# Performance work log

Hardware: AMD Instinct MI355X
Metric: run time of the kernel (lower is better)

The kernel has to match this reference:

```python
import jax, jax.numpy as jnp
import numpy as np

EPS = 1e-5

def _ln(t, g, b):
    m = t.mean(-1, keepdims=True)
    v = ((t - m) ** 2).mean(-1, keepdims=True)
    return (t - m) * jax.lax.rsqrt(v + EPS) * g + b

def _sr(t, w, b, H, W, sr):
    # t: [B, H*W, C] -> spatial-reduction conv -> [B, (H//sr)*(W//sr), C]
    B, L, C = t.shape
    xi = t.transpose(0, 2, 1).reshape(B, C, H, W)
    y = jax.lax.conv_general_dilated(xi, w, (sr, sr), 'VALID',
                                     dimension_numbers=('NCHW', 'OIHW', 'NCHW'))
    return y.reshape(B, C, -1).transpose(0, 2, 1) + b

def setup_inputs() -> dict:
    key = jax.random.key(0)
    ks = jax.random.split(key, 9)
    C, head, sr, H, W = 128, 2, 2, 64, 64
    B, N = 4, 2 * H * W
    s = 0.02
    return {
        'x': jax.random.normal(ks[0], (B, N, C), jnp.float32),
        'qW': jax.random.normal(ks[1], (C, C), jnp.float32) * s,
        'qb': jnp.zeros((C,), jnp.float32),
        'kvW': jax.random.normal(ks[2], (C, 2 * C), jnp.float32) * s,
        'kvb': jnp.zeros((2 * C,), jnp.float32),
        'projW': jax.random.normal(ks[3], (C, C), jnp.float32) * s,
        'projb': jnp.zeros((C,), jnp.float32),
        'srW': jax.random.normal(ks[4], (C, C, sr, sr), jnp.float32) * s,
        'srb': jnp.zeros((C,), jnp.float32),
        'lnW': jnp.ones((C,), jnp.float32),
        'lnB': jnp.zeros((C,), jnp.float32),
        'H': H, 'W': W, 'fuse': 1,
    }

def reference(x, qW, qb, kvW, kvb, projW, projb, srW, srb, lnW, lnB, H, W, fuse):
    head, sr = 2, 2
    B, N, C = x.shape
    Dh = C // head
    scale = Dh ** -0.5
    q = (x @ qW + qb).reshape(B, N, head, Dh).transpose(0, 2, 1, 3)  # [B,h,N,Dh]
    mask = None
    if fuse and sr > 1:
        half = N // 2
        x_rgb = _ln(_sr(x[:, :half, :], srW, srb, H, W, sr), lnW, lnB)
        x_dte = _ln(_sr(x[:, half:, :], srW, srb, H, W, sr), lnW, lnB)
        xkv = jnp.concatenate([x_rgb, x_dte], axis=1)
        M = N // (sr * sr)
        row = jnp.arange(N)[:, None] < half            # query in rgb half
        col = jnp.arange(M)[None, :] < (M // 2)        # key in rgb half
        mask = row == col                              # True on same-modality blocks -> masked
    elif sr > 1:
        xkv = _ln(_sr(x, srW, srb, H, W, sr), lnW, lnB)
    else:
        xkv = x
    M = xkv.shape[1]
    kv = (xkv @ kvW + kvb).reshape(B, M, 2, head, Dh).transpose(2, 0, 3, 1, 4)
    k, v = kv[0], kv[1]                                # [B,h,M,Dh]
    attn = jnp.einsum('bhnd,bhmd->bhnm', q, k) * scale
    if mask is not None:
        attn = jnp.where(mask[None, None], -jnp.inf, attn)
    attn = jax.nn.softmax(attn, axis=-1)
    out = jnp.einsum('bhnm,bhmd->bhnd', attn, v).transpose(0, 2, 1, 3).reshape(B, N, C)
    return out @ projW + projb
```

## Files before the change

### kernel.cpp

```cpp
#include <hip/hip_runtime.h>
#include <hip/hip_bf16.h>

#define LN_EPS 1e-5f

typedef __attribute__((ext_vector_type(8))) short bf16x8_t;
typedef __attribute__((ext_vector_type(4))) float f32x4_t;
typedef __attribute__((ext_vector_type(4))) unsigned short u16x4_t;

__device__ inline unsigned short f2bf(float f) {
    union { float f; unsigned int u; } v; v.f = f;
    unsigned int r = v.u + 0x7fffu + ((v.u >> 16) & 1u);
    return (unsigned short)(r >> 16);
}

__device__ inline size_t fragidx(int row, int k, int KC) {
    return ((size_t)((row >> 4) * KC + (k >> 5))) * 512 +
           (((k >> 3) & 3) * 16 + (row & 15)) * 8 + (k & 7);
}

__global__ void k_prep_w(const float* __restrict__ qW, const float* __restrict__ kvW,
                         const float* __restrict__ projW, const float* __restrict__ srW,
                         unsigned short* __restrict__ qWs, unsigned short* __restrict__ kvWs,
                         unsigned short* __restrict__ projWs, unsigned short* __restrict__ srWs) {
    int i = blockIdx.x * 256 + threadIdx.x;
    if (i < 16384) {
        int n = i & 127, k = i >> 7;
        qWs[fragidx(n, k, 4)] = f2bf(qW[k * 128 + n]);
    } else if (i < 49152) {
        int j = i - 16384; int n = j & 255, k = j >> 8;
        kvWs[fragidx(n, k, 4)] = f2bf(kvW[k * 256 + n]);
    } else if (i < 65536) {
        int j = i - 49152; int n = j & 127, k = j >> 7;
        projWs[fragidx(n, k, 4)] = f2bf(projW[k * 128 + n]);
    } else {
        int j = i - 65536; int n = j >> 9, rem = j & 511, q = rem >> 7, c = rem & 127;
        srWs[fragidx(n, q * 128 + c, 16)] = f2bf(srW[n * 512 + c * 4 + q]);
    }
}

__global__ void k_prep_x(const float* __restrict__ x, unsigned short* __restrict__ xsw,
                         unsigned short* __restrict__ Psw) {
    int i = blockIdx.x * 256 + threadIdx.x;
    int c4 = i & 31;
    int row = i >> 5;
    float4 v = *(const float4*)(x + (size_t)row * 128 + c4 * 4);
    u16x4_t o = { f2bf(v.x), f2bf(v.y), f2bf(v.z), f2bf(v.w) };
    int ch = c4 * 4;
    *(u16x4_t*)(xsw + fragidx(row, ch, 4)) = o;
    int b = row >> 13, n = row & 8191;
    int hf = n >> 12, rem = n & 4095;
    int y = rem >> 6, xc = rem & 63;
    int oy = y >> 1, ky = y & 1, ox = xc >> 1, kx = xc & 1;
    int q = ky * 2 + kx;
    int pos = b * 2048 + hf * 1024 + oy * 32 + ox;
    *(u16x4_t*)(Psw + fragidx(pos, q * 128 + ch, 16)) = o;
}

template <int RT, int KD, int NC, int MODE>
__global__ __launch_bounds__(256)
void k_gemm(const unsigned short* __restrict__ A, const unsigned short* __restrict__ W,
            const float* __restrict__ bias, void* __restrict__ out0,
            void* __restrict__ out1) {
    constexpr int KC = KD / 32;
    const int t = threadIdx.x, w = t >> 6, lane = t & 63;
    const int col = lane & 15, quad = lane >> 4;
    const int rt0 = blockIdx.y * RT;
    const int ct0 = blockIdx.x * 8 + w * 2;
    const unsigned short* ap = A + (size_t)rt0 * KC * 512 + lane * 8;
    const unsigned short* wp = W + (size_t)ct0 * KC * 512 + lane * 8;
    f32x4_t acc[RT][2] = {};
    #pragma unroll
    for (int kc = 0; kc < KC; kc++) {
        bf16x8_t b0 = *(const bf16x8_t*)(wp + (size_t)(0 * KC + kc) * 512);
        bf16x8_t b1 = *(const bf16x8_t*)(wp + (size_t)(1 * KC + kc) * 512);
        #pragma unroll
        for (int rt = 0; rt < RT; rt++) {
            bf16x8_t af = *(const bf16x8_t*)(ap + (size_t)(rt * KC + kc) * 512);
            acc[rt][0] = __builtin_amdgcn_mfma_f32_16x16x32_bf16(af, b0, acc[rt][0], 0, 0, 0);
            acc[rt][1] = __builtin_amdgcn_mfma_f32_16x16x32_bf16(af, b1, acc[rt][1], 0, 0, 0);
        }
    }
    #pragma unroll
    for (int rt = 0; rt < RT; rt++) {
        #pragma unroll
        for (int ct = 0; ct < 2; ct++) {
            int cc = (ct0 + ct) * 16 + col;
            float bs = bias[cc];
            float vals[4];
            #pragma unroll
            for (int r = 0; r < 4; r++) vals[r] = acc[rt][ct][r] + bs;
            int gr0 = (rt0 + rt) * 16 + quad * 4;
            if (MODE == 0) {
                #pragma unroll
                for (int r = 0; r < 4; r++)
                    ((float*)out0)[(size_t)(gr0 + r) * NC + cc] = vals[r];
            } else if (MODE == 1) {
                int d = cc & 63;
                #pragma unroll
                for (int r = 0; r < 4; r++) {
                    int gr = gr0 + r;
                    int bh = (gr >> 13) * 2 + (cc >> 6), n = gr & 8191;
                    ((unsigned short*)out0)[((size_t)((bh * 512 + (n >> 4)) * 2 + (d >> 5))) * 512 +
                                            (((d >> 3) & 3) * 16 + (n & 15)) * 8 + (d & 7)] =
                        f2bf(vals[r] * 0.125f);
                }
            } else {
                int b = gr0 >> 11;
                if (cc < 128) {
                    int bh = b * 2 + (cc >> 6), d = cc & 63;
                    #pragma unroll
                    for (int r = 0; r < 4; r++) {
                        int m = (gr0 + r) & 2047;
                        ((unsigned short*)out0)[((size_t)((bh * 128 + (m >> 4)) * 2 + (d >> 5))) * 512 +
                                                (((d >> 3) & 3) * 16 + (m & 15)) * 8 + (d & 7)] =
                            f2bf(vals[r]);
                    }
                } else {
                    int c2 = cc - 128;
                    int bh = b * 2 + (c2 >> 6), d = c2 & 63;
                    int m0 = gr0 & 2047;
                    u16x4_t o = { f2bf(vals[0]), f2bf(vals[1]), f2bf(vals[2]), f2bf(vals[3]) };
                    *(u16x4_t*)((unsigned short*)out1 +
                                ((size_t)((bh * 4 + (d >> 4)) * 64 + (m0 >> 5))) * 512 +
                                (((m0 >> 3) & 3) * 16 + (d & 15)) * 8 + (m0 & 7)) = o;
                }
            }
        }
    }
}

__global__ void k_ln(const float* __restrict__ Xp, const float* __restrict__ lnW,
                     const float* __restrict__ lnB, unsigned short* __restrict__ Ysw) {
    int t = threadIdx.x;
    int lane = t & 31;
    int row = blockIdx.x * 8 + (t >> 5);
    float4 v = ((const float4*)(Xp + (size_t)row * 128))[lane];
    float s = v.x + v.y + v.z + v.w;
    float ss = v.x * v.x + v.y * v.y + v.z * v.z + v.w * v.w;
    #pragma unroll
    for (int m = 16; m >= 1; m >>= 1) {
        s += __shfl_xor(s, m, 32);
        ss += __shfl_xor(ss, m, 32);
    }
    float mean = s * (1.0f / 128.0f);
    float var = ss * (1.0f / 128.0f) - mean * mean;
    float rs = rsqrtf(var + LN_EPS);
    float4 g = ((const float4*)lnW)[lane];
    float4 be = ((const float4*)lnB)[lane];
    u16x4_t o = { f2bf((v.x - mean) * rs * g.x + be.x),
                  f2bf((v.y - mean) * rs * g.y + be.y),
                  f2bf((v.z - mean) * rs * g.z + be.z),
                  f2bf((v.w - mean) * rs * g.w + be.w) };
    *(u16x4_t*)(Ysw + fragidx(row, lane * 4, 4)) = o;
}

__global__ __launch_bounds__(256, 2)
void k_attn3(const unsigned short* __restrict__ qsw,
             const unsigned short* __restrict__ ksw,
             const unsigned short* __restrict__ vsw,
             unsigned short* __restrict__ aoutsw) {
    const int bh = blockIdx.z, mod = blockIdx.y, bx = blockIdx.x;
    const int t = threadIdx.x, w = t >> 6, lane = t & 63;
    const int col = lane & 15, quad = lane >> 4;
    const int qbase = mod * 4096 + bx * 128 + w * 32;

    __shared__ unsigned short pp[4][2][16][72];

    bf16x8_t qf[2][2];
    {
        const unsigned short* qp =
            qsw + ((size_t)(bh * 512 + (qbase >> 4)) * 2) * 512 + lane * 8;
        qf[0][0] = *(const bf16x8_t*)(qp);
        qf[0][1] = *(const bf16x8_t*)(qp + 512);
        qf[1][0] = *(const bf16x8_t*)(qp + 1024);
        qf[1][1] = *(const bf16x8_t*)(qp + 1536);
    }
    const unsigned short* kp0 =
        ksw + ((size_t)(bh * 128 + (1 - mod) * 64) * 2) * 512 + lane * 8;
    const unsigned short* vp0 =
        vsw + ((size_t)(bh * 4) * 64 + (1 - mod) * 32) * 512 + lane * 8;

    const bf16x8_t ones = { 0x3F80, 0x3F80, 0x3F80, 0x3F80,
                            0x3F80, 0x3F80, 0x3F80, 0x3F80 };

    f32x4_t O[2][4] = {};
    f32x4_t accl[2] = {};

    bf16x8_t kcur[8];
    #pragma unroll
    for (int i = 0; i < 8; i++)
        kcur[i] = *(const bf16x8_t*)(kp0 + (size_t)i * 512);

    for (int kt = 0; kt < 16; kt++) {
        bf16x8_t vcur[8];
        #pragma unroll
        for (int dt = 0; dt < 4; dt++) {
            vcur[dt * 2 + 0] = *(const bf16x8_t*)(vp0 + ((size_t)dt * 64 + kt * 2 + 0) * 512);
            vcur[dt * 2 + 1] = *(const bf16x8_t*)(vp0 + ((size_t)dt * 64 + kt * 2 + 1) * 512);
        }
        const int ktn = (kt + 1) & 15;
        bf16x8_t knext[8];
        #pragma unroll
        for (int i = 0; i < 8; i++)
            knext[i] = *(const bf16x8_t*)(kp0 + (size_t)(ktn * 8 + i) * 512);

        f32x4_t ST[2][4];
        #pragma unroll
        for (int qt = 0; qt < 2; qt++)
            #pragma unroll
            for (int nb = 0; nb < 4; nb++) {
                f32x4_t s = {};
                s = __builtin_amdgcn_mfma_f32_16x16x32_bf16(kcur[nb * 2 + 0], qf[qt][0], s, 0, 0, 0);
                s = __builtin_amdgcn_mfma_f32_16x16x32_bf16(kcur[nb * 2 + 1], qf[qt][1], s, 0, 0, 0);
                ST[qt][nb] = s;
            }
        #pragma unroll
        for (int qt = 0; qt < 2; qt++)
            #pragma unroll
            for (int nb = 0; nb < 4; nb++) {
                u16x4_t pk = { f2bf(__expf(ST[qt][nb][0])), f2bf(__expf(ST[qt][nb][1])),
                               f2bf(__expf(ST[qt][nb][2])), f2bf(__expf(ST[qt][nb][3])) };
                *(u16x4_t*)(&pp[w][qt][col][nb * 16 + quad * 4]) = pk;
            }
        bf16x8_t pb[2][2];
        #pragma unroll
        for (int qt = 0; qt < 2; qt++) {
            pb[qt][0] = *(const bf16x8_t*)(&pp[w][qt][col][quad * 8]);
            pb[qt][1] = *(const bf16x8_t*)(&pp[w][qt][col][32 + quad * 8]);
        }
        #pragma unroll
        for (int qt = 0; qt < 2; qt++) {
            accl[qt] = __builtin_amdgcn_mfma_f32_16x16x32_bf16(ones, pb[qt][0], accl[qt], 0, 0, 0);
            accl[qt] = __builtin_amdgcn_mfma_f32_16x16x32_bf16(ones, pb[qt][1], accl[qt], 0, 0, 0);
        }
        #pragma unroll
        for (int dt = 0; dt < 4; dt++)
            #pragma unroll
            for (int qt = 0; qt < 2; qt++) {
                O[qt][dt] = __builtin_amdgcn_mfma_f32_16x16x32_bf16(vcur[dt * 2 + 0], pb[qt][0],
                                                                   O[qt][dt], 0, 0, 0);
                O[qt][dt] = __builtin_amdgcn_mfma_f32_16x16x32_bf16(vcur[dt * 2 + 1], pb[qt][1],
                                                                   O[qt][dt], 0, 0, 0);
            }
        #pragma unroll
        for (int i = 0; i < 8; i++) kcur[i] = knext[i];
    }

    const int b = bh >> 1, h = bh & 1;
    #pragma unroll
    for (int qt = 0; qt < 2; qt++) {
        float rl = 1.0f / accl[qt][0];
        int n_g = b * 8192 + qbase + qt * 16 + col;
        int rt_a = n_g >> 4;
        #pragma unroll
        for (int dt = 0; dt < 4; dt++) {
            int kc_a = h * 2 + (dt >> 1);
            int quad_a = (dt & 1) * 2 + (quad >> 1);
            int j0 = (quad & 1) * 4;
            u16x4_t o = { f2bf(O[qt][dt][0] * rl), f2bf(O[qt][dt][1] * rl),
                          f2bf(O[qt][dt][2] * rl), f2bf(O[qt][dt][3] * rl) };
            *(u16x4_t*)(aoutsw + ((size_t)(rt_a * 4 + kc_a)) * 512 +
                        (quad_a * 16 + col) * 8 + j0) = o;
        }
    }
}

extern "C" void kernel_launch(void* const* d_in, const int* in_sizes, int n_in,
                              void* d_out, int out_size, void* d_ws, size_t ws_size,
                              hipStream_t stream) {
    const float* x     = (const float*)d_in[0];
    const float* qW    = (const float*)d_in[1];
    const float* qb    = (const float*)d_in[2];
    const float* kvW   = (const float*)d_in[3];
    const float* kvb   = (const float*)d_in[4];
    const float* projW = (const float*)d_in[5];
    const float* projb = (const float*)d_in[6];
    const float* srW   = (const float*)d_in[7];
    const float* srb   = (const float*)d_in[8];
    const float* lnW   = (const float*)d_in[9];
    const float* lnB   = (const float*)d_in[10];

    char* ws = (char*)d_ws;
    unsigned short* qWs    = (unsigned short*)(ws + 0);
    unsigned short* kvWs   = (unsigned short*)(ws + 32768);
    unsigned short* projWs = (unsigned short*)(ws + 98304);
    unsigned short* srWs   = (unsigned short*)(ws + 131072);
    unsigned short* xsw    = (unsigned short*)(ws + 262144);
    unsigned short* Psw    = (unsigned short*)(ws + 8650752);
    unsigned short* qsw    = (unsigned short*)(ws + 17039360);
    unsigned short* ksw    = (unsigned short*)(ws + 25427968);
    unsigned short* vsw    = (unsigned short*)(ws + 27525120);
    float*          xkvp   = (float*)(ws + 29622272);
    unsigned short* xkvsw  = (unsigned short*)(ws + 33816576);
    unsigned short* aoutsw = (unsigned short*)(ws + 35913728);

    k_prep_w<<<dim3(512), dim3(256), 0, stream>>>(qW, kvW, projW, srW,
                                                  qWs, kvWs, projWs, srWs);
    k_prep_x<<<dim3(4096), dim3(256), 0, stream>>>(x, xsw, Psw);
    k_gemm<4, 128, 128, 1><<<dim3(1, 512), dim3(256), 0, stream>>>(xsw, qWs, qb,
                                                                   (void*)qsw, nullptr);
    k_gemm<2, 512, 128, 0><<<dim3(1, 256), dim3(256), 0, stream>>>(Psw, srWs, srb,
                                                                   (void*)xkvp, nullptr);
    k_ln<<<dim3(1024), dim3(256), 0, stream>>>(xkvp, lnW, lnB, xkvsw);
    k_gemm<2, 128, 256, 2><<<dim3(2, 256), dim3(256), 0, stream>>>(xkvsw, kvWs, kvb,
                                                                   (void*)ksw, (void*)vsw);
    k_attn3<<<dim3(32, 2, 8), dim3(256), 0, stream>>>(qsw, ksw, vsw, aoutsw);
    k_gemm<4, 128, 128, 0><<<dim3(1, 512), dim3(256), 0, stream>>>(aoutsw, projWs, projb,
                                                                   d_out, nullptr);
}
```

Measured before the change: 157.2 us.

## Transpose GEMMs to compute full rows per wave, fuse LayerNorm into SR GEMM

Reworks the projection GEMMs so the weight operand is the MFMA A-side and each wave owns all 128 output channels for two row tiles. This lets the spatial-reduction GEMM apply LayerNorm in registers and drop the separate fp32 intermediate and LN kernel, and it allows vectorized float4/u16x4 stores. The V projection gets its own small kernel. Softmax switches to exp2 with log2e folded into the q scale, and bf16 packing uses hardware conversion intrinsics. The trade-off is fewer blocks (64–256) with large accumulator arrays, which may lower occupancy.

Measured after the change: 190.5 us. 21.2% more time.

```diff
diff --git a/kernel.cpp b/kernel.cpp
--- a/kernel.cpp
+++ b/kernel.cpp
@@ -11,6 +11,13 @@
     union { float f; unsigned int u; } v; v.f = f;
     unsigned int r = v.u + 0x7fffu + ((v.u >> 16) & 1u);
     return (unsigned short)(r >> 16);
+}
+
+__device__ inline u16x4_t pk4(float a, float b, float c, float d) {
+    union { u16x4_t v; __hip_bfloat162 h[2]; } u;
+    u.h[0] = __float22bfloat162_rn(float2{a, b});
+    u.h[1] = __float22bfloat162_rn(float2{c, d});
+    return u.v;
 }
 
 __device__ inline size_t fragidx(int row, int k, int KC) {
@@ -44,7 +51,7 @@
     int c4 = i & 31;
     int row = i >> 5;
     float4 v = *(const float4*)(x + (size_t)row * 128 + c4 * 4);
-    u16x4_t o = { f2bf(v.x), f2bf(v.y), f2bf(v.z), f2bf(v.w) };
+    u16x4_t o = pk4(v.x, v.y, v.z, v.w);
     int ch = c4 * 4;
     *(u16x4_t*)(xsw + fragidx(row, ch, 4)) = o;
     int b = row >> 13, n = row & 8191;
@@ -56,102 +63,137 @@
     *(u16x4_t*)(Psw + fragidx(pos, q * 128 + ch, 16)) = o;
 }
 
-template <int RT, int KD, int NC, int MODE>
+template <int KC, int MODE>
 __global__ __launch_bounds__(256)
-void k_gemm(const unsigned short* __restrict__ A, const unsigned short* __restrict__ W,
-            const float* __restrict__ bias, void* __restrict__ out0,
-            void* __restrict__ out1) {
-    constexpr int KC = KD / 32;
+void k_gemmT(const unsigned short* __restrict__ Wf, const unsigned short* __restrict__ Xf,
+             const float* __restrict__ bias, const float* __restrict__ lnW,
+             const float* __restrict__ lnB, void* __restrict__ out) {
     const int t = threadIdx.x, w = t >> 6, lane = t & 63;
     const int col = lane & 15, quad = lane >> 4;
-    const int rt0 = blockIdx.y * RT;
-    const int ct0 = blockIdx.x * 8 + w * 2;
-    const unsigned short* ap = A + (size_t)rt0 * KC * 512 + lane * 8;
-    const unsigned short* wp = W + (size_t)ct0 * KC * 512 + lane * 8;
-    f32x4_t acc[RT][2] = {};
+    const int rt0 = blockIdx.x * 8 + w * 2;
+    const unsigned short* xp = Xf + (size_t)rt0 * KC * 512 + lane * 8;
+    const unsigned short* wp = Wf + lane * 8;
+    f32x4_t acc[8][2] = {};
     #pragma unroll
     for (int kc = 0; kc < KC; kc++) {
-        bf16x8_t b0 = *(const bf16x8_t*)(wp + (size_t)(0 * KC + kc) * 512);
-        bf16x8_t b1 = *(const bf16x8_t*)(wp + (size_t)(1 * KC + kc) * 512);
-        #pragma unroll
-        for (int rt = 0; rt < RT; rt++) {
-            bf16x8_t af = *(const bf16x8_t*)(ap + (size_t)(rt * KC + kc) * 512);
-            acc[rt][0] = __builtin_amdgcn_mfma_f32_16x16x32_bf16(af, b0, acc[rt][0], 0, 0, 0);
-            acc[rt][1] = __builtin_amdgcn_mfma_f32_16x16x32_bf16(af, b1, acc[rt][1], 0, 0, 0);
-        }
-    }
-    #pragma unroll
-    for (int rt = 0; rt < RT; rt++) {
+        bf16x8_t x0 = *(const bf16x8_t*)(xp + (size_t)kc * 512);
+        bf16x8_t x1 = *(const bf16x8_t*)(xp + (size_t)(KC + kc) * 512);
+        #pragma unroll
+        for (int nt = 0; nt < 8; nt++) {
+            bf16x8_t wf = *(const bf16x8_t*)(wp + (size_t)(nt * KC + kc) * 512);
+            acc[nt][0] = __builtin_amdgcn_mfma_f32_16x16x32_bf16(wf, x0, acc[nt][0], 0, 0, 0);
+            acc[nt][1] = __builtin_amdgcn_mfma_f32_16x16x32_bf16(wf, x1, acc[nt][1], 0, 0, 0);
+        }
+    }
+    if constexpr (MODE == 3) {
+        #pragma unroll
+        for (int nt = 0; nt < 8; nt++) {
+            float4 bs = *(const float4*)(bias + nt * 16 + quad * 4);
+            #pragma unroll
+            for (int ct = 0; ct < 2; ct++) {
+                acc[nt][ct][0] += bs.x; acc[nt][ct][1] += bs.y;
+                acc[nt][ct][2] += bs.z; acc[nt][ct][3] += bs.w;
+            }
+        }
         #pragma unroll
         for (int ct = 0; ct < 2; ct++) {
-            int cc = (ct0 + ct) * 16 + col;
-            float bs = bias[cc];
-            float vals[4];
-            #pragma unroll
-            for (int r = 0; r < 4; r++) vals[r] = acc[rt][ct][r] + bs;
-            int gr0 = (rt0 + rt) * 16 + quad * 4;
-            if (MODE == 0) {
-                #pragma unroll
-                for (int r = 0; r < 4; r++)
-                    ((float*)out0)[(size_t)(gr0 + r) * NC + cc] = vals[r];
-            } else if (MODE == 1) {
-                int d = cc & 63;
+            float s = 0.f, ss = 0.f;
+            #pragma unroll
+            for (int nt = 0; nt < 8; nt++)
                 #pragma unroll
                 for (int r = 0; r < 4; r++) {
-                    int gr = gr0 + r;
-                    int bh = (gr >> 13) * 2 + (cc >> 6), n = gr & 8191;
-                    ((unsigned short*)out0)[((size_t)((bh * 512 + (n >> 4)) * 2 + (d >> 5))) * 512 +
-                                            (((d >> 3) & 3) * 16 + (n & 15)) * 8 + (d & 7)] =
-                        f2bf(vals[r] * 0.125f);
+                    float v = acc[nt][ct][r];
+                    s += v; ss += v * v;
                 }
-            } else {
-                int b = gr0 >> 11;
-                if (cc < 128) {
-                    int bh = b * 2 + (cc >> 6), d = cc & 63;
-                    #pragma unroll
-                    for (int r = 0; r < 4; r++) {
-                        int m = (gr0 + r) & 2047;
-                        ((unsigned short*)out0)[((size_t)((bh * 128 + (m >> 4)) * 2 + (d >> 5))) * 512 +
-                                                (((d >> 3) & 3) * 16 + (m & 15)) * 8 + (d & 7)] =
-                            f2bf(vals[r]);
-                    }
+            s += __shfl_xor(s, 16, 64);  s += __shfl_xor(s, 32, 64);
+            ss += __shfl_xor(ss, 16, 64); ss += __shfl_xor(ss, 32, 64);
+            float mean = s * (1.0f / 128.0f);
+            float var = ss * (1.0f / 128.0f) - mean * mean;
+            float rs = rsqrtf(var + LN_EPS);
+            int p = (rt0 + ct) * 16 + col;
+            #pragma unroll
+            for (int nt = 0; nt < 8; nt++) {
+                float4 g = *(const float4*)(lnW + nt * 16 + quad * 4);
+                float4 be = *(const float4*)(lnB + nt * 16 + quad * 4);
+                u16x4_t o = pk4((acc[nt][ct][0] - mean) * rs * g.x + be.x,
+                                (acc[nt][ct][1] - mean) * rs * g.y + be.y,
+                                (acc[nt][ct][2] - mean) * rs * g.z + be.z,
+                                (acc[nt][ct][3] - mean) * rs * g.w + be.w);
+                *(u16x4_t*)((unsigned short*)out +
+                            ((size_t)((p >> 4) * 4 + (nt >> 1))) * 512 +
+                            (((nt & 1) * 2 + (quad >> 1)) * 16 + (p & 15)) * 8 +
+                            (quad & 1) * 4) = o;
+            }
+        }
+    } else {
+        #pragma unroll
+        for (int nt = 0; nt < 8; nt++) {
+            float4 bs = *(const float4*)(bias + nt * 16 + quad * 4);
+            #pragma unroll
+            for (int ct = 0; ct < 2; ct++) {
+                int p = (rt0 + ct) * 16 + col;
+                float v0 = acc[nt][ct][0] + bs.x, v1 = acc[nt][ct][1] + bs.y;
+                float v2 = acc[nt][ct][2] + bs.z, v3 = acc[nt][ct][3] + bs.w;
+                if (MODE == 0) {
+                    float4 o = { v0, v1, v2, v3 };
+                    *(float4*)((float*)out + (size_t)p * 128 + nt * 16 + quad * 4) = o;
+                } else if (MODE == 1) {
+                    const float sc = 0.125f * 1.44269504089f;
+                    int bh = (p >> 13) * 2 + (nt >> 2), n = p & 8191;
+                    u16x4_t o = pk4(v0 * sc, v1 * sc, v2 * sc, v3 * sc);
+                    *(u16x4_t*)((unsigned short*)out +
+                                ((size_t)(bh * 512 + (n >> 4)) * 2 + ((nt >> 1) & 1)) * 512 +
+                                (((nt & 1) * 2 + (quad >> 1)) * 16 + (n & 15)) * 8 +
+                                (quad & 1) * 4) = o;
                 } else {
-                    int c2 = cc - 128;
-                    int bh = b * 2 + (c2 >> 6), d = c2 & 63;
-                    int m0 = gr0 & 2047;
-                    u16x4_t o = { f2bf(vals[0]), f2bf(vals[1]), f2bf(vals[2]), f2bf(vals[3]) };
-                    *(u16x4_t*)((unsigned short*)out1 +
-                                ((size_t)((bh * 4 + (d >> 4)) * 64 + (m0 >> 5))) * 512 +
-                                (((m0 >> 3) & 3) * 16 + (d & 15)) * 8 + (m0 & 7)) = o;
+                    int bh = (p >> 11) * 2 + (nt >> 2), m = p & 2047;
+                    u16x4_t o = pk4(v0, v1, v2, v3);
+                    *(u16x4_t*)((unsigned short*)out +
+                                ((size_t)(bh * 128 + (m >> 4)) * 2 + ((nt >> 1) & 1)) * 512 +
+                                (((nt & 1) * 2 + (quad >> 1)) * 16 + (m & 15)) * 8 +
+                                (quad & 1) * 4) = o;
                 }
             }
         }
     }
 }
 
-__global__ void k_ln(const float* __restrict__ Xp, const float* __restrict__ lnW,
-                     const float* __restrict__ lnB, unsigned short* __restrict__ Ysw) {
-    int t = threadIdx.x;
-    int lane = t & 31;
-    int row = blockIdx.x * 8 + (t >> 5);
-    float4 v = ((const float4*)(Xp + (size_t)row * 128))[lane];
-    float s = v.x + v.y + v.z + v.w;
-    float ss = v.x * v.x + v.y * v.y + v.z * v.z + v.w * v.w;
-    #pragma unroll
-    for (int m = 16; m >= 1; m >>= 1) {
-        s += __shfl_xor(s, m, 32);
-        ss += __shfl_xor(ss, m, 32);
-    }
-    float mean = s * (1.0f / 128.0f);
-    float var = ss * (1.0f / 128.0f) - mean * mean;
-    float rs = rsqrtf(var + LN_EPS);
-    float4 g = ((const float4*)lnW)[lane];
-    float4 be = ((const float4*)lnB)[lane];
-    u16x4_t o = { f2bf((v.x - mean) * rs * g.x + be.x),
-                  f2bf((v.y - mean) * rs * g.y + be.y),
-                  f2bf((v.z - mean) * rs * g.z + be.z),
-                  f2bf((v.w - mean) * rs * g.w + be.w) };
-    *(u16x4_t*)(Ysw + fragidx(row, lane * 4, 4)) = o;
+__global__ __launch_bounds__(256)
+void k_gemmV(const unsigned short* __restrict__ Xf, const unsigned short* __restrict__ kvWs,
+             const float* __restrict__ kvb, unsigned short* __restrict__ vsw) {
+    const int t = threadIdx.x, w = t >> 6, lane = t & 63;
+    const int col = lane & 15, quad = lane >> 4;
+    const int rt0 = blockIdx.x * 2;
+    const unsigned short* ap = Xf + (size_t)rt0 * 4 * 512 + lane * 8;
+    const unsigned short* wp = kvWs + (size_t)(8 + w * 2) * 4 * 512 + lane * 8;
+    f32x4_t acc[2][2] = {};
+    #pragma unroll
+    for (int kc = 0; kc < 4; kc++) {
+        bf16x8_t a0 = *(const bf16x8_t*)(ap + (size_t)kc * 512);
+        bf16x8_t a1 = *(const bf16x8_t*)(ap + (size_t)(4 + kc) * 512);
+        bf16x8_t b0 = *(const bf16x8_t*)(wp + (size_t)kc * 512);
+        bf16x8_t b1 = *(const bf16x8_t*)(wp + (size_t)(4 + kc) * 512);
+        acc[0][0] = __builtin_amdgcn_mfma_f32_16x16x32_bf16(a0, b0, acc[0][0], 0, 0, 0);
+        acc[0][1] = __builtin_amdgcn_mfma_f32_16x16x32_bf16(a0, b1, acc[0][1], 0, 0, 0);
+        acc[1][0] = __builtin_amdgcn_mfma_f32_16x16x32_bf16(a1, b0, acc[1][0], 0, 0, 0);
+        acc[1][1] = __builtin_amdgcn_mfma_f32_16x16x32_bf16(a1, b1, acc[1][1], 0, 0, 0);
+    }
+    #pragma unroll
+    for (int rt = 0; rt < 2; rt++) {
+        #pragma unroll
+        for (int ct = 0; ct < 2; ct++) {
+            int d = (w * 2 + ct) * 16 + col;
+            int h = d >> 6, dd = d & 63;
+            float bs = kvb[128 + d];
+            int gr0 = (rt0 + rt) * 16 + quad * 4;
+            int b = gr0 >> 11, m0 = gr0 & 2047;
+            int bh = b * 2 + h, dt = dd >> 4;
+            u16x4_t o = pk4(acc[rt][ct][0] + bs, acc[rt][ct][1] + bs,
+                            acc[rt][ct][2] + bs, acc[rt][ct][3] + bs);
+            *(u16x4_t*)(vsw + ((size_t)((bh * 4 + dt) * 64 + (m0 >> 5))) * 512 +
+                        (((m0 >> 3) & 3) * 16 + (dd & 15)) * 8 + (m0 & 7)) = o;
+        }
+    }
 }
 
 __global__ __launch_bounds__(256, 2)
@@ -218,8 +260,8 @@
         for (int qt = 0; qt < 2; qt++)
             #pragma unroll
             for (int nb = 0; nb < 4; nb++) {
-                u16x4_t pk = { f2bf(__expf(ST[qt][nb][0])), f2bf(__expf(ST[qt][nb][1])),
-                               f2bf(__expf(ST[qt][nb][2])), f2bf(__expf(ST[qt][nb][3])) };
+                u16x4_t pk = pk4(exp2f(ST[qt][nb][0]), exp2f(ST[qt][nb][1]),
+                                 exp2f(ST[qt][nb][2]), exp2f(ST[qt][nb][3]));
                 *(u16x4_t*)(&pp[w][qt][col][nb * 16 + quad * 4]) = pk;
             }
         bf16x8_t pb[2][2];
@@ -257,8 +299,8 @@
             int kc_a = h * 2 + (dt >> 1);
             int quad_a = (dt & 1) * 2 + (quad >> 1);
             int j0 = (quad & 1) * 4;
-            u16x4_t o = { f2bf(O[qt][dt][0] * rl), f2bf(O[qt][dt][1] * rl),
-                          f2bf(O[qt][dt][2] * rl), f2bf(O[qt][dt][3] * rl) };
+            u16x4_t o = pk4(O[qt][dt][0] * rl, O[qt][dt][1] * rl,
+                            O[qt][dt][2] * rl, O[qt][dt][3] * rl);
             *(u16x4_t*)(aoutsw + ((size_t)(rt_a * 4 + kc_a)) * 512 +
                         (quad_a * 16 + col) * 8 + j0) = o;
         }
@@ -290,21 +332,20 @@
     unsigned short* qsw    = (unsigned short*)(ws + 17039360);
     unsigned short* ksw    = (unsigned short*)(ws + 25427968);
     unsigned short* vsw    = (unsigned short*)(ws + 27525120);
-    float*          xkvp   = (float*)(ws + 29622272);
-    unsigned short* xkvsw  = (unsigned short*)(ws + 33816576);
-    unsigned short* aoutsw = (unsigned short*)(ws + 35913728);
+    unsigned short* xkvsw  = (unsigned short*)(ws + 29622272);
+    unsigned short* aoutsw = (unsigned short*)(ws + 31719424);
 
     k_prep_w<<<dim3(512), dim3(256), 0, stream>>>(qW, kvW, projW, srW,
                                                   qWs, kvWs, projWs, srWs);
     k_prep_x<<<dim3(4096), dim3(256), 0, stream>>>(x, xsw, Psw);
-    k_gemm<4, 128, 128, 1><<<dim3(1, 512), dim3(256), 0, stream>>>(xsw, qWs, qb,
-                                                                   (void*)qsw, nullptr);
-    k_gemm<2, 512, 128, 0><<<dim3(1, 256), dim3(256), 0, stream>>>(Psw, srWs, srb,
-                                                                   (void*)xkvp, nullptr);
-    k_ln<<<dim3(1024), dim3(256), 0, stream>>>(xkvp, lnW, lnB, xkvsw);
-    k_gemm<2, 128, 256, 2><<<dim3(2, 256), dim3(256), 0, stream>>>(xkvsw, kvWs, kvb,
-                                                                   (void*)ksw, (void*)vsw);
+    k_gemmT<4, 1><<<dim3(256), dim3(256), 0, stream>>>(qWs, xsw, qb, nullptr, nullptr,
+                                                       (void*)qsw);
+    k_gemmT<16, 3><<<dim3(64), dim3(256), 0, stream>>>(srWs, Psw, srb, lnW, lnB,
+                                                       (void*)xkvsw);
+    k_gemmT<4, 2><<<dim3(64), dim3(256), 0, stream>>>(kvWs, xkvsw, kvb, nullptr, nullptr,
+                                                      (void*)ksw);
+    k_gemmV<<<dim3(256), dim3(256), 0, stream>>>(xkvsw, kvWs, kvb, vsw);
     k_attn3<<<dim3(32, 2, 8), dim3(256), 0, stream>>>(qsw, ksw, vsw, aoutsw);
-    k_gemm<4, 128, 128, 0><<<dim3(1, 512), dim3(256), 0, stream>>>(aoutsw, projWs, projb,
-                                                                   d_out, nullptr);
-}
+    k_gemmT<4, 0><<<dim3(256), dim3(256), 0, stream>>>(projWs, aoutsw, projb, nullptr,
+                                                       nullptr, d_out);
+}
```
